# Performance work log

Measured on AMD Instinct MI355X. Metric: run time of the kernel, lower is better.

## Reference

```python
import jax, jax.numpy as jnp
import numpy as np

EPS = 1e-10


def setup_inputs() -> dict:
    key = jax.random.key(0)
    k_logits, k_temp, k_exp = jax.random.split(key, 3)
    B, V = 256, 128000
    logits = jax.random.normal(k_logits, (B, V), dtype=jnp.float32)
    temperatures = jax.random.uniform(k_temp, (B,), dtype=jnp.float32, minval=0.1, maxval=2.0)
    # first quarter of rows are greedy (temperature == 0), as in the torch.where branch
    temperatures = temperatures.at[: B // 4].set(0.0)
    # single exponential(1) noise row of shape (vocab,), expanded across batch in the kernel
    exponential = jax.random.exponential(k_exp, (V,), dtype=jnp.float32)
    return {"logits": logits, "temperatures": temperatures, "exponential": exponential}


def reference(logits, temperatures, exponential):
    # logits: [B, V] fp32, temperatures: [B], exponential: [V] shared across rows
    logits = logits.astype(jnp.float32)
    greedy = temperatures == 0.0                      # [B]
    safe_t = jnp.where(greedy, 1.0, temperatures)      # avoid div-by-zero on greedy rows
    # temperature-scaled softmax, single stable pass
    probs = jax.nn.softmax(logits / safe_t[:, None], axis=-1)  # [B, V]
    # Gumbel-max via exponential noise: argmax(p / E) ~ Categorical(p)
    noisy = probs / (exponential[None, :] + EPS)       # [B, V]
    scores = jnp.where(greedy[:, None], logits, noisy) # greedy rows: raw argmax
    sampled_tokens = jnp.argmax(scores, axis=-1).astype(jnp.int32)  # [B]
    return sampled_tokens
```

## Files before the change

### kernel.cpp

```cpp
#include <hip/hip_runtime.h>
#include <hip/hip_bf16.h>
#include <math.h>

#define EPS 1e-10f
#define LOG2E 1.4426950408889634f

typedef float floatx4 __attribute__((ext_vector_type(4)));

__global__ __launch_bounds__(1024) void sampler_row_kernel(
    const float* __restrict__ logits,
    const float* __restrict__ temps,
    const float* __restrict__ expo,
    int* __restrict__ out, int V) {

    const int row = blockIdx.x;
    const float t = temps[row];
    const bool greedy = (t == 0.0f);
    const float c = greedy ? 1.0f : (LOG2E / t);

    const float*   rl  = logits + (size_t)row * (size_t)V;
    const floatx4* rl4 = reinterpret_cast<const floatx4*>(rl);
    const floatx4* e4  = reinterpret_cast<const floatx4*>(expo);

    float best = -INFINITY;
    int   bidx = 0x7fffffff;

    const int nvec = V >> 2;

    if (greedy) {
        for (int i = threadIdx.x; i < nvec; i += 1024) {
            floatx4 l = rl4[i];
            int base = i << 2;
            if (l.x > best) { best = l.x; bidx = base;     }
            if (l.y > best) { best = l.y; bidx = base + 1; }
            if (l.z > best) { best = l.z; bidx = base + 2; }
            if (l.w > best) { best = l.w; bidx = base + 3; }
        }
    } else {
        for (int i = threadIdx.x; i < nvec; i += 1024) {
            floatx4 l = rl4[i];
            floatx4 e = e4[i];
            float s0 = fmaf(l.x, c, -__builtin_amdgcn_logf(e.x + EPS));
            float s1 = fmaf(l.y, c, -__builtin_amdgcn_logf(e.y + EPS));
            float s2 = fmaf(l.z, c, -__builtin_amdgcn_logf(e.z + EPS));
            float s3 = fmaf(l.w, c, -__builtin_amdgcn_logf(e.w + EPS));
            int base = i << 2;
            if (s0 > best) { best = s0; bidx = base;     }
            if (s1 > best) { best = s1; bidx = base + 1; }
            if (s2 > best) { best = s2; bidx = base + 2; }
            if (s3 > best) { best = s3; bidx = base + 3; }
        }
    }

    for (int j = (nvec << 2) + threadIdx.x; j < V; j += 1024) {
        float s = greedy ? rl[j]
                         : fmaf(rl[j], c, -__builtin_amdgcn_logf(expo[j] + EPS));
        if (s > best) { best = s; bidx = j; }
    }

    #pragma unroll
    for (int off = 32; off >= 1; off >>= 1) {
        float ov = __shfl_down(best, off);
        int   oi = __shfl_down(bidx, off);
        if (ov > best || (ov == best && oi < bidx)) { best = ov; bidx = oi; }
    }

    __shared__ float sv[16];
    __shared__ int   si[16];
    const int wid  = threadIdx.x >> 6;
    const int lane = threadIdx.x & 63;
    if (lane == 0) { sv[wid] = best; si[wid] = bidx; }
    __syncthreads();

    if (wid == 0) {
        best = (lane < 16) ? sv[lane] : -INFINITY;
        bidx = (lane < 16) ? si[lane] : 0x7fffffff;
        #pragma unroll
        for (int off = 8; off >= 1; off >>= 1) {
            float ov = __shfl_down(best, off);
            int   oi = __shfl_down(bidx, off);
            if (ov > best || (ov == best && oi < bidx)) { best = ov; bidx = oi; }
        }
        if (lane == 0) out[row] = bidx;
    }
}

extern "C" void kernel_launch(void* const* d_in, const int* in_sizes, int n_in,
                              void* d_out, int out_size, void* d_ws, size_t ws_size,
                              hipStream_t stream) {
    const float* logits = (const float*)d_in[0];
    const float* temps  = (const float*)d_in[1];
    const float* expo   = (const float*)d_in[2];
    int*         out    = (int*)d_out;

    const int B = in_sizes[1];
    const int V = in_sizes[2];

    sampler_row_kernel<<<B, 1024, 0, stream>>>(logits, temps, expo, out, V);
}
```

Baseline: 26.01 us.

## Split each row across two blocks with atomic 64-bit key argmax merge

Each row is now handled by two blocks, each scanning half the vocabulary. The blocks merge through an atomicMax on a packed key of order-preserving float bits and inverted index kept in workspace, and the last block to finish (found through an atomic counter) writes the outputs. This doubles the grid to raise parallelism and memory-level concurrency across CUs, at the cost of a memset launch, global atomics and a serial tail in the last block. The original per-row kernel stays as a fallback when the workspace is too small.

After: 44.42 us. 1.71x slower.

```diff
diff --git a/kernel.cpp b/kernel.cpp
--- a/kernel.cpp
+++ b/kernel.cpp
@@ -7,13 +7,23 @@
 
 typedef float floatx4 __attribute__((ext_vector_type(4)));
 
-__global__ __launch_bounds__(1024) void sampler_row_kernel(
+__device__ __forceinline__ unsigned int ordf(float f) {
+    unsigned int b = __float_as_uint(f);
+    return (b & 0x80000000u) ? ~b : (b | 0x80000000u);
+}
+
+__global__ __launch_bounds__(1024) void sampler_split_kernel(
     const float* __restrict__ logits,
     const float* __restrict__ temps,
     const float* __restrict__ expo,
-    int* __restrict__ out, int V) {
+    int* __restrict__ out,
+    unsigned long long* __restrict__ keys,
+    unsigned int* __restrict__ ctr,
+    int B, int V, int halfLen) {
 
-    const int row = blockIdx.x;
+    const int row  = blockIdx.x >> 1;
+    const int half = blockIdx.x & 1;
+
     const float t = temps[row];
     const bool greedy = (t == 0.0f);
     const float c = greedy ? 1.0f : (LOG2E / t);
@@ -22,37 +32,37 @@
     const floatx4* rl4 = reinterpret_cast<const floatx4*>(rl);
     const floatx4* e4  = reinterpret_cast<const floatx4*>(expo);
 
+    const int beg  = half * halfLen;
+    const int end  = min(beg + halfLen, V);
+    const int beg4 = beg >> 2;
+    const int end4 = end >> 2;
+
     float best = -INFINITY;
     int   bidx = 0x7fffffff;
 
-    const int nvec = V >> 2;
-
     if (greedy) {
-        for (int i = threadIdx.x; i < nvec; i += 1024) {
-            floatx4 l = rl4[i];
-            int base = i << 2;
-            if (l.x > best) { best = l.x; bidx = base;     }
-            if (l.y > best) { best = l.y; bidx = base + 1; }
-            if (l.z > best) { best = l.z; bidx = base + 2; }
-            if (l.w > best) { best = l.w; bidx = base + 3; }
+        for (int i = beg4 + threadIdx.x; i < end4; i += 1024) {
+            floatx4 a = rl4[i];
+            int ab = i << 2;
+            if (a.x > best) { best = a.x; bidx = ab;     }
+            if (a.y > best) { best = a.y; bidx = ab + 1; }
+            if (a.z > best) { best = a.z; bidx = ab + 2; }
+            if (a.w > best) { best = a.w; bidx = ab + 3; }
         }
     } else {
-        for (int i = threadIdx.x; i < nvec; i += 1024) {
-            floatx4 l = rl4[i];
-            floatx4 e = e4[i];
-            float s0 = fmaf(l.x, c, -__builtin_amdgcn_logf(e.x + EPS));
-            float s1 = fmaf(l.y, c, -__builtin_amdgcn_logf(e.y + EPS));
-            float s2 = fmaf(l.z, c, -__builtin_amdgcn_logf(e.z + EPS));
-            float s3 = fmaf(l.w, c, -__builtin_amdgcn_logf(e.w + EPS));
-            int base = i << 2;
-            if (s0 > best) { best = s0; bidx = base;     }
-            if (s1 > best) { best = s1; bidx = base + 1; }
-            if (s2 > best) { best = s2; bidx = base + 2; }
-            if (s3 > best) { best = s3; bidx = base + 3; }
+        for (int i = beg4 + threadIdx.x; i < end4; i += 1024) {
+            floatx4 a  = rl4[i];
+            floatx4 ea = e4[i];
+            int ab = i << 2;
+            float s;
+            s = fmaf(a.x, c, -__builtin_amdgcn_logf(ea.x + EPS)); if (s > best) { best = s; bidx = ab;     }
+            s = fmaf(a.y, c, -__builtin_amdgcn_logf(ea.y + EPS)); if (s > best) { best = s; bidx = ab + 1; }
+            s = fmaf(a.z, c, -__builtin_amdgcn_logf(ea.z + EPS)); if (s > best) { best = s; bidx = ab + 2; }
+            s = fmaf(a.w, c, -__builtin_amdgcn_logf(ea.w + EPS)); if (s > best) { best = s; bidx = ab + 3; }
         }
     }
 
-    for (int j = (nvec << 2) + threadIdx.x; j < V; j += 1024) {
+    for (int j = (end4 << 2) + threadIdx.x; j < ((half == 1) ? V : 0); j += 1024) {
         float s = greedy ? rl[j]
                          : fmaf(rl[j], c, -__builtin_amdgcn_logf(expo[j] + EPS));
         if (s > best) { best = s; bidx = j; }
@@ -72,6 +82,79 @@
     if (lane == 0) { sv[wid] = best; si[wid] = bidx; }
     __syncthreads();
 
+    if (threadIdx.x == 0) {
+        best = sv[0]; bidx = si[0];
+        #pragma unroll
+        for (int w = 1; w < 16; ++w) {
+            if (sv[w] > best || (sv[w] == best && si[w] < bidx)) { best = sv[w]; bidx = si[w]; }
+        }
+        unsigned long long key =
+            ((unsigned long long)ordf(best) << 32) | (unsigned int)(~bidx);
+        atomicMax(&keys[row], key);
+    }
+
+    __shared__ int sLast;
+    if (threadIdx.x == 0) {
+        __threadfence();
+        unsigned int old = atomicAdd(ctr, 1u);
+        sLast = (old == (unsigned int)(gridDim.x - 1)) ? 1 : 0;
+    }
+    __syncthreads();
+    if (sLast) {
+        for (int r = threadIdx.x; r < B; r += 1024) {
+            unsigned long long k = atomicMax(&keys[r], 0ULL);
+            out[r] = (int)(~(unsigned int)(k & 0xFFFFFFFFull));
+        }
+    }
+}
+
+__global__ __launch_bounds__(1024) void sampler_row_kernel(
+    const float* __restrict__ logits,
+    const float* __restrict__ temps,
+    const float* __restrict__ expo,
+    int* __restrict__ out, int V) {
+    const int row = blockIdx.x;
+    const float t = temps[row];
+    const bool greedy = (t == 0.0f);
+    const float c = greedy ? 1.0f : (LOG2E / t);
+    const float*   rl  = logits + (size_t)row * (size_t)V;
+    const floatx4* rl4 = reinterpret_cast<const floatx4*>(rl);
+    const floatx4* e4  = reinterpret_cast<const floatx4*>(expo);
+    float best = -INFINITY; int bidx = 0x7fffffff;
+    const int nvec = V >> 2;
+    for (int i = threadIdx.x; i < nvec; i += 1024) {
+        floatx4 l = rl4[i];
+        float s0, s1, s2, s3;
+        if (greedy) { s0 = l.x; s1 = l.y; s2 = l.z; s3 = l.w; }
+        else {
+            floatx4 e = e4[i];
+            s0 = fmaf(l.x, c, -__builtin_amdgcn_logf(e.x + EPS));
+            s1 = fmaf(l.y, c, -__builtin_amdgcn_logf(e.y + EPS));
+            s2 = fmaf(l.z, c, -__builtin_amdgcn_logf(e.z + EPS));
+            s3 = fmaf(l.w, c, -__builtin_amdgcn_logf(e.w + EPS));
+        }
+        int base = i << 2;
+        if (s0 > best) { best = s0; bidx = base;     }
+        if (s1 > best) { best = s1; bidx = base + 1; }
+        if (s2 > best) { best = s2; bidx = base + 2; }
+        if (s3 > best) { best = s3; bidx = base + 3; }
+    }
+    for (int j = (nvec << 2) + threadIdx.x; j < V; j += 1024) {
+        float s = greedy ? rl[j]
+                         : fmaf(rl[j], c, -__builtin_amdgcn_logf(expo[j] + EPS));
+        if (s > best) { best = s; bidx = j; }
+    }
+    #pragma unroll
+    for (int off = 32; off >= 1; off >>= 1) {
+        float ov = __shfl_down(best, off);
+        int   oi = __shfl_down(bidx, off);
+        if (ov > best || (ov == best && oi < bidx)) { best = ov; bidx = oi; }
+    }
+    __shared__ float sv[16];
+    __shared__ int   si[16];
+    const int wid = threadIdx.x >> 6, lane = threadIdx.x & 63;
+    if (lane == 0) { sv[wid] = best; si[wid] = bidx; }
+    __syncthreads();
     if (wid == 0) {
         best = (lane < 16) ? sv[lane] : -INFINITY;
         bidx = (lane < 16) ? si[lane] : 0x7fffffff;
@@ -96,5 +179,16 @@
     const int B = in_sizes[1];
     const int V = in_sizes[2];
 
-    sampler_row_kernel<<<B, 1024, 0, stream>>>(logits, temps, expo, out, V);
+    const int halfLen = (((V + 1) / 2) + 3) & ~3;
+    const size_t need = (size_t)B * 8 + 64;
+
+    if (ws_size >= need) {
+        unsigned long long* keys = (unsigned long long*)d_ws;
+        unsigned int* ctr = (unsigned int*)((char*)d_ws + (size_t)B * 8);
+        hipMemsetAsync(d_ws, 0, need, stream);
+        sampler_split_kernel<<<2 * B, 1024, 0, stream>>>(
+            logits, temps, expo, out, keys, ctr, B, V, halfLen);
+    } else {
+        sampler_row_kernel<<<B, 1024, 0, stream>>>(logits, temps, expo, out, V);
+    }
 }
```
